# Performance work log

Measured on AMD Instinct MI355X. Metric: run time of the kernel, lower is better.

The kernel has to match this reference:

```python
import jax, jax.numpy as jnp
import numpy as np

N = 50000
E = 800000
IN_C = 256
NHID = 32
HEADS = 4
OUT_C = 64
HID = NHID * HEADS  # 128
SLOPE = 0.2


def setup_inputs() -> dict:
    key = jax.random.key(0)
    ks = jax.random.split(key, 16)
    s = lambda *d: 1.0 / np.sqrt(d[0])
    inp = {
        "x": jax.random.normal(ks[0], (N, IN_C), dtype=jnp.float32),
        "edge_index": jax.random.randint(ks[1], (2, E), 0, N, dtype=jnp.int64),
        # conv1: GATConv(IN_C, NHID, heads=HEADS, concat=True)
        "W1": jax.random.normal(ks[2], (IN_C, HEADS * NHID), dtype=jnp.float32) * s(IN_C),
        "att_src1": jax.random.normal(ks[3], (HEADS, NHID), dtype=jnp.float32) * s(NHID),
        "att_dst1": jax.random.normal(ks[4], (HEADS, NHID), dtype=jnp.float32) * s(NHID),
        "b1": jnp.zeros((HEADS * NHID,), dtype=jnp.float32),
        # conv2: GATConv(HID, OUT_C, heads=1, concat=False)
        "W2": jax.random.normal(ks[5], (HID, OUT_C), dtype=jnp.float32) * s(HID),
        "att_src2": jax.random.normal(ks[6], (1, OUT_C), dtype=jnp.float32) * s(OUT_C),
        "att_dst2": jax.random.normal(ks[7], (1, OUT_C), dtype=jnp.float32) * s(OUT_C),
        "b2": jnp.zeros((OUT_C,), dtype=jnp.float32),
        # res1: Linear(IN_C, HID)
        "res1_w": jax.random.normal(ks[8], (IN_C, HID), dtype=jnp.float32) * s(IN_C),
        "res1_b": jnp.zeros((HID,), dtype=jnp.float32),
        # fc: Linear(HID, OUT_C)
        "fc_w": jax.random.normal(ks[9], (HID, OUT_C), dtype=jnp.float32) * s(HID),
        "fc_b": jnp.zeros((OUT_C,), dtype=jnp.float32),
    }
    return inp


def leaky_relu(x, slope=SLOPE):
    return jnp.where(x >= 0, x, slope * x)


def gat_conv(x, edge_index, W, att_src, att_dst, bias, heads, out_c, concat):
    """PyG GATConv with default add_self_loops=True, negative_slope=0.2."""
    n = x.shape[0]
    loop = jnp.arange(n, dtype=edge_index.dtype)
    src = jnp.concatenate([edge_index[0], loop])  # [E+N]
    dst = jnp.concatenate([edge_index[1], loop])
    h = (x @ W).reshape(n, heads, out_c)          # [N,H,C]
    a_src = (h * att_src[None]).sum(-1)           # [N,H]
    a_dst = (h * att_dst[None]).sum(-1)
    alpha = leaky_relu(a_src[src] + a_dst[dst])   # [E+N,H]
    # segment softmax over destination nodes (every node has a self loop)
    amax = jax.ops.segment_max(alpha, dst, num_segments=n)
    expa = jnp.exp(alpha - amax[dst])
    denom = jax.ops.segment_sum(expa, dst, num_segments=n)
    alpha = expa / (denom[dst] + 1e-16)
    msg = alpha[:, :, None] * h[src]              # [E+N,H,C] irregular gather
    out = jax.ops.segment_sum(msg, dst, num_segments=n)  # scatter-add
    if concat:
        out = out.reshape(n, heads * out_c)
    else:
        out = out.mean(axis=1)
    return out + bias


def reference(x, edge_index, W1, att_src1, att_dst1, b1, W2, att_src2, att_dst2, b2,
              res1_w, res1_b, fc_w, fc_b):
    x_res = x @ res1_w + res1_b
    h = gat_conv(x, edge_index, W1, att_src1, att_dst1, b1, HEADS, NHID, True) + x_res
    h_res = h @ fc_w + fc_b
    h = leaky_relu(h)
    z = gat_conv(h, edge_index, W2, att_src2, att_dst2, b2, 1, OUT_C, False) + h_res
    z = leaky_relu(z)
    return z
```

## Files before the change

### kernel.cpp

```cpp
#include <hip/hip_runtime.h>

typedef __attribute__((ext_vector_type(8))) short short8;
typedef __attribute__((ext_vector_type(4))) float f32x4;

constexpr int BCAP = 4096;

__device__ __forceinline__ ushort rne_bf16(float f) {
  uint u = __float_as_uint(f);
  uint r = (u + 0x7FFFu + ((u >> 16) & 1u)) >> 16;
  return (ushort)r;
}
__device__ __forceinline__ float bf16_lo(uint pair) { return __uint_as_float(pair << 16); }
__device__ __forceinline__ float bf16_hi(uint pair) { return __uint_as_float(pair & 0xffff0000u); }
__device__ __forceinline__ float bf1(ushort v) { return __uint_as_float((uint)v << 16); }
__device__ __forceinline__ float lrelu(float a) { return a >= 0.f ? a : 0.2f * a; }

__device__ __forceinline__ uint lrelu_pair(uint pair) {
  float lo = lrelu(bf16_lo(pair));
  float hi = lrelu(bf16_hi(pair));
  return (uint)rne_bf16(lo) | ((uint)rne_bf16(hi) << 16);
}
__device__ __forceinline__ float4 lrelu_bf8(float4 v) {
  uint4 u = *(uint4*)&v;
  u.x = lrelu_pair(u.x); u.y = lrelu_pair(u.y);
  u.z = lrelu_pair(u.z); u.w = lrelu_pair(u.w);
  return *(float4*)&u;
}
__device__ __forceinline__ float4 pack_bf8(float4 a, float4 b) {
  uint u0 = (uint)rne_bf16(a.x) | ((uint)rne_bf16(a.y) << 16);
  uint u1 = (uint)rne_bf16(a.z) | ((uint)rne_bf16(a.w) << 16);
  uint u2 = (uint)rne_bf16(b.x) | ((uint)rne_bf16(b.y) << 16);
  uint u3 = (uint)rne_bf16(b.z) | ((uint)rne_bf16(b.w) << 16);
  uint4 r; r.x = u0; r.y = u1; r.z = u2; r.w = u3;
  return *(float4*)&r;
}

__global__ __launch_bounds__(256) void prep_all_k(
    const int* __restrict__ ei, int E, int nEB,
    int* __restrict__ bcnt, uint2* __restrict__ tmp, int nbuck,
    const float* __restrict__ W1, const float* __restrict__ res1_w,
    const float* __restrict__ fc_w, const float* __restrict__ W2,
    ushort* __restrict__ Wt1, ushort* __restrict__ fcT, ushort* __restrict__ W2T)
{
  __shared__ int lcnt[400];
  __shared__ int gbase[400];
  const int tid = threadIdx.x, bid = blockIdx.x;
  const long gstride = (long)gridDim.x * 256;
  const long g0 = (long)bid * 256 + tid;

  if (bid < nEB) {
    for (int i = tid; i < nbuck; i += 256) lcnt[i] = 0;
    __syncthreads();
    const int ebase = bid * 4096;
    int srcs[16], dsts[16], rk[16];
#pragma unroll
    for (int i = 0; i < 16; ++i) {
      int e = ebase + i * 256 + tid;
      if (e < E) {
        srcs[i] = ei[e];
        dsts[i] = ei[E + e];
        rk[i] = atomicAdd(&lcnt[dsts[i] >> 7], 1);
      } else dsts[i] = -1;
    }
    __syncthreads();
    for (int b = tid; b < nbuck; b += 256)
      gbase[b] = lcnt[b] ? atomicAdd(&bcnt[b], lcnt[b]) : 0;
    __syncthreads();
#pragma unroll
    for (int i = 0; i < 16; ++i) {
      if (dsts[i] >= 0) {
        int b = dsts[i] >> 7;
        tmp[(size_t)b * BCAP + gbase[b] + rk[i]] = make_uint2((uint)srcs[i], (uint)dsts[i]);
      }
    }
  }

  for (long gi = g0; gi < 81920; gi += gstride) {
    const float* src; ushort* dst; int K, NO; long local;
    if (gi < 32768)            { src = W1;     dst = Wt1;          K = 256; NO = 128; local = gi; }
    else if (gi < 65536)       { src = res1_w; dst = Wt1 + 32768;  K = 256; NO = 128; local = gi - 32768; }
    else if (gi < 65536+8192)  { src = fc_w;   dst = fcT;          K = 128; NO = 64;  local = gi - 65536; }
    else                       { src = W2;     dst = W2T;          K = 128; NO = 64;  local = gi - 65536 - 8192; }
    int n = (int)(local / K), k = (int)(local % K);
    dst[local] = rne_bf16(src[(size_t)k * NO + n]);
  }
}

__global__ __launch_bounds__(512) void scan_buckets_k(const int* __restrict__ bcnt,
                                                      int* __restrict__ bbase,
                                                      int* __restrict__ offp,
                                                      int nbuck, int N) {
  __shared__ int sh[512];
  int tid = threadIdx.x;
  int v = (tid < nbuck) ? bcnt[tid] : 0;
  sh[tid] = v;
  __syncthreads();
  for (int o = 1; o < 512; o <<= 1) {
    int t = (tid >= o) ? sh[tid - o] : 0;
    __syncthreads();
    sh[tid] += t;
    __syncthreads();
  }
  if (tid < nbuck) bbase[tid] = sh[tid] - v;
  if (tid == nbuck - 1) { bbase[nbuck] = sh[tid]; offp[N] = sh[tid]; }
}

__global__ __launch_bounds__(512) void gemm1_k(
    const float* __restrict__ x, const ushort* __restrict__ Wt1,
    const float* __restrict__ res1_b,
    const float* __restrict__ att_s1, const float* __restrict__ att_d1,
    ushort* __restrict__ h1bf, ushort* __restrict__ xresbf,
    float* __restrict__ a_s, float* __restrict__ a_d,
    const uint2* __restrict__ tmp, const int* __restrict__ bcnt,
    const int* __restrict__ bbase, int* __restrict__ offp,
    int* __restrict__ csr, int nbuck, int M)
{
  constexpr int LDA = 72;
  __shared__ ushort smem[64 * LDA + 128 * LDA];
  const int bid = blockIdx.x, y = blockIdx.y, tid = threadIdx.x;
  ushort* As = smem;
  ushort* Bs = smem + 64 * LDA;
  const int w = tid >> 6, l = tid & 63;
  const int wr = w >> 2, wc = w & 3;
  const int l15 = l & 15, lg = l >> 4;
  const int row0 = bid * 64;
  const int srow = tid >> 3, sch = tid & 7;

  int gra = row0 + srow; if (gra >= M) gra = M - 1;
  const float*  Apf = x + (size_t)gra * 256 + sch * 8;
  const ushort* Bp  = Wt1 + ((size_t)y * 128 + srow) * 256 + sch * 8;

  f32x4 acc[2][2] = {};
  float4 raCa, raCb, rbC0, rbC1, raNa, raNb, rbN0, rbN1;
  raCa = *(const float4*)(Apf);
  raCb = *(const float4*)(Apf + 4);
  rbC0 = *(const float4*)(Bp);
  rbC1 = *(const float4*)(Bp + 64 * 256);

#pragma unroll
  for (int kt = 0; kt < 4; ++kt) {
    __syncthreads();
    *(float4*)&As[srow * LDA + sch * 8] = pack_bf8(raCa, raCb);
    *(float4*)&Bs[srow * LDA + sch * 8] = rbC0;
    *(float4*)&Bs[(64 + srow) * LDA + sch * 8] = rbC1;
    __syncthreads();
    if (kt < 3) {
      int k1 = (kt + 1) * 64;
      raNa = *(const float4*)(Apf + k1);
      raNb = *(const float4*)(Apf + k1 + 4);
      rbN0 = *(const float4*)(Bp + k1);
      rbN1 = *(const float4*)(Bp + 64 * 256 + k1);
    }
    short8 aF[2][2], bF[2][2];
#pragma unroll
    for (int m = 0; m < 2; ++m)
#pragma unroll
      for (int kk = 0; kk < 2; ++kk)
        aF[m][kk] = *(const short8*)&As[(wr * 32 + m * 16 + l15) * LDA + kk * 32 + lg * 8];
#pragma unroll
    for (int n = 0; n < 2; ++n)
#pragma unroll
      for (int kk = 0; kk < 2; ++kk)
        bF[n][kk] = *(const short8*)&Bs[(wc * 32 + n * 16 + l15) * LDA + kk * 32 + lg * 8];
#pragma unroll
    for (int m = 0; m < 2; ++m)
#pragma unroll
      for (int n = 0; n < 2; ++n)
#pragma unroll
        for (int kk = 0; kk < 2; ++kk)
          acc[m][n] = __builtin_amdgcn_mfma_f32_16x16x32_bf16(aF[m][kk], bF[n][kk], acc[m][n], 0, 0, 0);
    raCa = raNa; raCb = raNb; rbC0 = rbN0; rbC1 = rbN1;
  }
  __syncthreads();

  ushort* Cs = smem;
#pragma unroll
  for (int m = 0; m < 2; ++m)
#pragma unroll
    for (int n = 0; n < 2; ++n)
#pragma unroll
      for (int j = 0; j < 4; ++j) {
        int rl = wr * 32 + m * 16 + lg * 4 + j;
        int col = wc * 32 + n * 16 + l15;
        float v = acc[m][n][j] + (y ? res1_b[col] : 0.f);
        Cs[rl * 128 + col] = rne_bf16(v);
      }
  __syncthreads();

  if (y == 0) {
    int r = tid >> 3, s = tid & 7, h = s >> 1;
    int gr = row0 + r;
    float ps = 0.f, pd = 0.f;
#pragma unroll
    for (int i = 0; i < 16; ++i) {
      int col = s * 16 + i;
      float v = bf1(Cs[r * 128 + col]);
      ps += v * att_s1[h * 32 + (col & 31)];
      pd += v * att_d1[h * 32 + (col & 31)];
    }
    ps += __shfl_xor(ps, 1, 64);
    pd += __shfl_xor(pd, 1, 64);
    if (!(s & 1) && gr < M) { a_s[gr * 4 + h] = ps; a_d[gr * 4 + h] = pd; }
  }

  {
    ushort* out = y ? xresbf : h1bf;
#pragma unroll
    for (int idx = tid; idx < 1024; idx += 512) {
      int row = idx >> 4, c16 = idx & 15;
      int gr = row0 + row;
      if (gr < M)
        *(uint4*)&out[(size_t)gr * 128 + c16 * 8] = *(const uint4*)&Cs[row * 128 + c16 * 8];
    }
  }

  if (y == 1 && bid < nbuck) {
    __syncthreads();
    int* lcnt = (int*)smem;
    int* excl = lcnt + 128;
    const int vbase = bid * 128;
    const int nloc = ((vbase + 128 < M) ? 128 : M - vbase);
    const int cntb = bcnt[bid];
    const int bbase0 = bbase[bid];
    const uint2* bt = tmp + (size_t)bid * BCAP;
    if (tid < 128) lcnt[tid] = 0;
    __syncthreads();
    for (int e = tid; e < cntb; e += 512)
      atomicAdd(&lcnt[(int)bt[e].y - vbase], 1);
    __syncthreads();
    if (tid < 128) {
      int v = lcnt[tid];
      int sc = v;
#pragma unroll
      for (int o = 1; o < 64; o <<= 1) {
        int t = __shfl_up(sc, o, 64);
        if ((tid & 63) >= o) sc += t;
      }
      excl[tid] = sc - v;
    }
    __syncthreads();
    if (tid >= 64 && tid < 128) excl[tid] += excl[63] + lcnt[63];
    __syncthreads();
    if (tid < nloc) offp[vbase + tid] = bbase0 + excl[tid];
    if (tid < 128) lcnt[tid] = 0;
    __syncthreads();
    for (int e = tid; e < cntb; e += 512) {
      uint2 t = bt[e];
      int li = (int)t.y - vbase;
      int r = atomicAdd(&lcnt[li], 1);
      csr[bbase0 + excl[li] + r] = (int)t.x;
    }
  }
}

__global__ __launch_bounds__(512) void gemm2_k(
    const ushort* __restrict__ hpre,
    const ushort* __restrict__ fcT,
    const float* __restrict__ fc_b,
    const float* __restrict__ att_s2, const float* __restrict__ att_d2,
    ushort* __restrict__ hresb, ushort* __restrict__ h2bf,
    float* __restrict__ a_s, float* __restrict__ a_d, int M)
{
  constexpr int LDA = 72;
  __shared__ ushort smem[64 * LDA + 64 * LDA];
  const int tid = threadIdx.x, y = blockIdx.y;
  const ushort* B = fcT + (size_t)y * 64 * 128;
  ushort* out = y ? h2bf : hresb;
  const int row0 = blockIdx.x * 64;
  ushort* As = smem;
  ushort* Bs = smem + 64 * LDA;
  const int w = tid >> 6, l = tid & 63;
  const int wr = w >> 1, wc = w & 1;
  const int l15 = l & 15, lg = l >> 4;
  const int srow = tid >> 3, sch = tid & 7;

  int gra = row0 + srow; if (gra >= M) gra = M - 1;
  const ushort* Ap = hpre + (size_t)gra * 128 + sch * 8;
  const ushort* Bp = B + (size_t)srow * 128 + sch * 8;

  f32x4 acc[2] = {};
  float4 raC = *(const float4*)(Ap);
  float4 rbC = *(const float4*)(Bp);
  if (y) raC = lrelu_bf8(raC);
  float4 raN, rbN;

#pragma unroll
  for (int kt = 0; kt < 2; ++kt) {
    __syncthreads();
    *(float4*)&As[srow * LDA + sch * 8] = raC;
    *(float4*)&Bs[srow * LDA + sch * 8] = rbC;
    __syncthreads();
    if (kt < 1) {
      raN = *(const float4*)(Ap + 64);
      rbN = *(const float4*)(Bp + 64);
      if (y) raN = lrelu_bf8(raN);
    }

    short8 aF[2], bF[2][2];
#pragma unroll
    for (int kk = 0; kk < 2; ++kk)
      aF[kk] = *(const short8*)&As[(wr * 16 + l15) * LDA + kk * 32 + lg * 8];
#pragma unroll
    for (int n = 0; n < 2; ++n)
#pragma unroll
      for (int kk = 0; kk < 2; ++kk)
        bF[n][kk] = *(const short8*)&Bs[(wc * 32 + n * 16 + l15) * LDA + kk * 32 + lg * 8];
#pragma unroll
    for (int n = 0; n < 2; ++n)
#pragma unroll
      for (int kk = 0; kk < 2; ++kk)
        acc[n] = __builtin_amdgcn_mfma_f32_16x16x32_bf16(aF[kk], bF[n][kk], acc[n], 0, 0, 0);
    raC = raN; rbC = rbN;
  }
  __syncthreads();

  ushort* Cs = smem;
#pragma unroll
  for (int n = 0; n < 2; ++n)
#pragma unroll
    for (int j = 0; j < 4; ++j) {
      int rl = wr * 16 + lg * 4 + j;
      int col = wc * 32 + n * 16 + l15;
      float v = acc[n][j] + (y == 0 ? fc_b[col] : 0.f);
      Cs[rl * 64 + col] = rne_bf16(v);
    }
  __syncthreads();

  if (y == 1) {
    int r = tid >> 3, s = tid & 7;
    int gr = row0 + r;
    float ps = 0.f, pd = 0.f;
#pragma unroll
    for (int i = 0; i < 8; ++i) {
      int col = s * 8 + i;
      float v = bf1(Cs[r * 64 + col]);
      ps += v * att_s2[col];
      pd += v * att_d2[col];
    }
    ps += __shfl_xor(ps, 1, 64); pd += __shfl_xor(pd, 1, 64);
    ps += __shfl_xor(ps, 2, 64); pd += __shfl_xor(pd, 2, 64);
    ps += __shfl_xor(ps, 4, 64); pd += __shfl_xor(pd, 4, 64);
    if (s == 0 && gr < M) { a_s[gr] = ps; a_d[gr] = pd; }
  }

  {
    int row = tid >> 3, c16 = tid & 7;
    int gr = row0 + row;
    if (gr < M)
      *(uint4*)&out[(size_t)gr * 64 + c16 * 8] = *(const uint4*)&Cs[row * 64 + c16 * 8];
  }
}

__global__ __launch_bounds__(256) void aggr1_k(const uint* __restrict__ h1u,
                                               const uint* __restrict__ xresu,
                                               const float* __restrict__ a_s,
                                               const float* __restrict__ a_d,
                                               const int* __restrict__ off,
                                               const int* __restrict__ csr,
                                               const float* __restrict__ b1,
                                               uint* __restrict__ hpreu, int n) {
  int w = threadIdx.x >> 6, l = threadIdx.x & 63;
  int d = blockIdx.x * 4 + w;
  if (d >= n) return;
  int h = l >> 4, c = l * 2;
  int le = l & 15, hb = l & 48;
  float adh = a_d[d * 4 + h];
  float ws = __expf(lrelu(a_s[d * 4 + h] + adh));
  uint pd = h1u[(size_t)d * 64 + l];
  float lsum = ws, accx = ws * bf16_lo(pd), accy = ws * bf16_hi(pd);

  int s0 = off[d], s1 = off[d + 1];
  int p = s0;
  for (; p + 16 <= s1; p += 16) {
    int idxv = csr[p + le];
    float wv = __expf(lrelu(a_s[idxv * 4 + h] + adh));
    float wi[16]; int sv[16];
#pragma unroll
    for (int i = 0; i < 16; ++i) {
      wi[i] = __shfl(wv, hb + i, 64);
      sv[i] = __shfl(idxv, i, 64);
    }
#pragma unroll
    for (int i = 0; i < 16; ++i) {
      uint q = h1u[(size_t)sv[i] * 64 + l];
      lsum += wi[i];
      accx += wi[i] * bf16_lo(q);
      accy += wi[i] * bf16_hi(q);
    }
  }
  if (p < s1) {
    int rem = s1 - p;
    int jp = p + le;
    bool valid = jp < s1;
    int jc = valid ? jp : s1 - 1;
    int idxv = csr[jc];
    float wv = valid ? __expf(lrelu(a_s[idxv * 4 + h] + adh)) : 0.f;
    for (int i = 0; i < rem; i += 4) {
#pragma unroll
      for (int j = 0; j < 4; ++j) {
        float wib = __shfl(wv, hb + i + j, 64);
        int svb = __shfl(idxv, i + j, 64);
        uint q = h1u[(size_t)svb * 64 + l];
        lsum += wib;
        accx += wib * bf16_lo(q);
        accy += wib * bf16_hi(q);
      }
    }
  }
  float inv = 1.f / (lsum + 1e-16f);
  uint xr = xresu[(size_t)d * 64 + l];
  float vx = accx * inv + b1[c] + bf16_lo(xr);
  float vy = accy * inv + b1[c + 1] + bf16_hi(xr);
  hpreu[(size_t)d * 64 + l] = (uint)rne_bf16(vx) | ((uint)rne_bf16(vy) << 16);
}

__global__ __launch_bounds__(256) void aggr2_k(const ushort* __restrict__ h2b,
                                               const ushort* __restrict__ hresb,
                                               const float* __restrict__ a_s,
                                               const float* __restrict__ a_d,
                                               const int* __restrict__ off,
                                               const int* __restrict__ csr,
                                               const float* __restrict__ b2,
                                               float* __restrict__ out, int n) {
  int w = threadIdx.x >> 6, l = threadIdx.x & 63;
  int d = blockIdx.x * 4 + w;
  if (d >= n) return;
  int le = l & 15;
  float adh = a_d[d];
  float ws = __expf(lrelu(a_s[d] + adh));
  float lsum = ws;
  float acc = ws * bf1(h2b[(size_t)d * 64 + l]);

  int s0 = off[d], s1 = off[d + 1];
  int p = s0;
  for (; p + 16 <= s1; p += 16) {
    int idxv = csr[p + le];
    float wv = __expf(lrelu(a_s[idxv] + adh));
    float wi[16]; int sv[16];
#pragma unroll
    for (int i = 0; i < 16; ++i) {
      wi[i] = __shfl(wv, i, 64);
      sv[i] = __shfl(idxv, i, 64);
    }
#pragma unroll
    for (int i = 0; i < 16; ++i) {
      float fv = bf1(h2b[(size_t)sv[i] * 64 + l]);
      lsum += wi[i];
      acc += wi[i] * fv;
    }
  }
  if (p < s1) {
    int rem = s1 - p;
    int jp = p + le;
    bool valid = jp < s1;
    int jc = valid ? jp : s1 - 1;
    int idxv = csr[jc];
    float wv = valid ? __expf(lrelu(a_s[idxv] + adh)) : 0.f;
    for (int i = 0; i < rem; i += 4) {
#pragma unroll
      for (int j = 0; j < 4; ++j) {
        float wib = __shfl(wv, i + j, 64);
        int svb = __shfl(idxv, i + j, 64);
        float fv = bf1(h2b[(size_t)svb * 64 + l]);
        lsum += wib;
        acc += wib * fv;
      }
    }
  }
  float inv = 1.f / (lsum + 1e-16f);
  float z = acc * inv + b2[l] + bf1(hresb[(size_t)d * 64 + l]);
  out[(size_t)d * 64 + l] = lrelu(z);
}

extern "C" void kernel_launch(void* const* d_in, const int* in_sizes, int n_in,
                              void* d_out, int out_size, void* d_ws, size_t ws_size,
                              hipStream_t stream) {
  const float* x        = (const float*)d_in[0];
  const int*   ei       = (const int*)d_in[1];
  const float* W1       = (const float*)d_in[2];
  const float* att_src1 = (const float*)d_in[3];
  const float* att_dst1 = (const float*)d_in[4];
  const float* b1       = (const float*)d_in[5];
  const float* W2       = (const float*)d_in[6];
  const float* att_src2 = (const float*)d_in[7];
  const float* att_dst2 = (const float*)d_in[8];
  const float* b2       = (const float*)d_in[9];
  const float* res1_w   = (const float*)d_in[10];
  const float* res1_b   = (const float*)d_in[11];
  const float* fc_w     = (const float*)d_in[12];
  const float* fc_b     = (const float*)d_in[13];
  float* out = (float*)d_out;

  const int N = in_sizes[0] / 256;
  const int E = in_sizes[1] / 2;
  const int nbuck = (N + 127) / 128;
  const int nEB = (E + 4095) / 4096;

  ushort* h1bf   = (ushort*)d_ws;
  ushort* xresbf = h1bf + (size_t)N * 128;
  uint*   hpreu  = (uint*)(xresbf + (size_t)N * 128);
  float*  as1    = (float*)(hpreu + (size_t)N * 64);
  float*  ad1    = as1 + (size_t)N * 4;
  ushort* Wt1    = (ushort*)(ad1 + (size_t)N * 4);
  ushort* fcT    = Wt1 + 256 * 256;
  ushort* W2T    = fcT + 64 * 128;
  int* offp      = (int*)(W2T + 64 * 128);
  int* csr       = offp + N + 1;
  int* bcnt      = csr + E;
  int* bbase     = bcnt + 512;
  uint2* tmp     = (uint2*)(((uintptr_t)(bbase + 520) + 7) & ~(uintptr_t)7);
  ushort* h2bf   = h1bf;
  ushort* hresb  = xresbf;
  float*  as2 = as1, *ad2 = ad1;

  const int ngemm = (N + 63) / 64;

  hipMemsetAsync(bcnt, 0, 512 * 4, stream);
  prep_all_k<<<nEB, 256, 0, stream>>>(ei, E, nEB, bcnt, tmp, nbuck,
                                      W1, res1_w, fc_w, W2, Wt1, fcT, W2T);
  scan_buckets_k<<<1, 512, 0, stream>>>(bcnt, bbase, offp, nbuck, N);

  gemm1_k<<<dim3(ngemm, 2), 512, 0, stream>>>(x, Wt1, res1_b, att_src1, att_dst1,
                                              h1bf, xresbf, as1, ad1,
                                              tmp, bcnt, bbase, offp, csr, nbuck, N);

  aggr1_k<<<(N + 3) / 4, 256, 0, stream>>>((const uint*)h1bf, (const uint*)xresbf, as1, ad1,
                                           offp, csr, b1, hpreu, N);

  gemm2_k<<<dim3(ngemm, 2), 512, 0, stream>>>(
      (const ushort*)hpreu, fcT, fc_b,
      att_src2, att_dst2, hresb, h2bf, as2, ad2, N);

  aggr2_k<<<(N + 3) / 4, 256, 0, stream>>>(h2bf, hresb, as2, ad2, offp, csr, b2, out, N);
}
```

Baseline: 149.3 us.

## Fuse layer-1 aggregation into second GEMM via shared-memory hpre tile

Merges the layer-1 attention aggregation kernel with the second-layer GEMM. Each 512-thread block aggregates 64 destination nodes into a bf16 tile in shared memory, then runs both the fc and W2 products on that tile with MFMA. This removes the global write and re-read of the intermediate hpre buffer and one kernel launch. In exchange, occupancy for the irregular gather phase drops: 782 large blocks with a bigger shared-memory footprint replace 12500 small ones, and layer-2 outputs now need separate workspace buffers.

```diff
diff --git a/kernel.cpp b/kernel.cpp
--- a/kernel.cpp
+++ b/kernel.cpp
@@ -20,11 +20,11 @@
   float hi = lrelu(bf16_hi(pair));
   return (uint)rne_bf16(lo) | ((uint)rne_bf16(hi) << 16);
 }
-__device__ __forceinline__ float4 lrelu_bf8(float4 v) {
+__device__ __forceinline__ short8 lrelu_s8(short8 v) {
   uint4 u = *(uint4*)&v;
   u.x = lrelu_pair(u.x); u.y = lrelu_pair(u.y);
   u.z = lrelu_pair(u.z); u.w = lrelu_pair(u.w);
-  return *(float4*)&u;
+  return *(short8*)&u;
 }
 __device__ __forceinline__ float4 pack_bf8(float4 a, float4 b) {
   uint u0 = (uint)rne_bf16(a.x) | ((uint)rne_bf16(a.y) << 16);
@@ -253,165 +253,146 @@
   }
 }
 
-__global__ __launch_bounds__(512) void gemm2_k(
-    const ushort* __restrict__ hpre,
+__global__ __launch_bounds__(512) void agg1_gemm2_k(
+    const uint* __restrict__ h1u, const uint* __restrict__ xresu,
+    const float* __restrict__ a_s1, const float* __restrict__ a_d1,
+    const int* __restrict__ off, const int* __restrict__ csr,
+    const float* __restrict__ b1,
     const ushort* __restrict__ fcT,
     const float* __restrict__ fc_b,
     const float* __restrict__ att_s2, const float* __restrict__ att_d2,
     ushort* __restrict__ hresb, ushort* __restrict__ h2bf,
-    float* __restrict__ a_s, float* __restrict__ a_d, int M)
+    float* __restrict__ a_s2, float* __restrict__ a_d2, int n)
 {
-  constexpr int LDA = 72;
-  __shared__ ushort smem[64 * LDA + 64 * LDA];
-  const int tid = threadIdx.x, y = blockIdx.y;
-  const ushort* B = fcT + (size_t)y * 64 * 128;
-  ushort* out = y ? h2bf : hresb;
-  const int row0 = blockIdx.x * 64;
-  ushort* As = smem;
-  ushort* Bs = smem + 64 * LDA;
+  constexpr int LDH = 136;
+  __shared__ ushort smem[64 * LDH + 128 * LDH];
+  ushort* hpreT = smem;
+  ushort* Bs    = smem + 64 * LDH;
+
+  const int tid = threadIdx.x;
   const int w = tid >> 6, l = tid & 63;
-  const int wr = w >> 1, wc = w & 1;
   const int l15 = l & 15, lg = l >> 4;
-  const int srow = tid >> 3, sch = tid & 7;
-
-  int gra = row0 + srow; if (gra >= M) gra = M - 1;
-  const ushort* Ap = hpre + (size_t)gra * 128 + sch * 8;
-  const ushort* Bp = B + (size_t)srow * 128 + sch * 8;
-
-  f32x4 acc[2] = {};
-  float4 raC = *(const float4*)(Ap);
-  float4 rbC = *(const float4*)(Bp);
-  if (y) raC = lrelu_bf8(raC);
-  float4 raN, rbN;
-
-#pragma unroll
-  for (int kt = 0; kt < 2; ++kt) {
-    __syncthreads();
-    *(float4*)&As[srow * LDA + sch * 8] = raC;
-    *(float4*)&Bs[srow * LDA + sch * 8] = rbC;
-    __syncthreads();
-    if (kt < 1) {
-      raN = *(const float4*)(Ap + 64);
-      rbN = *(const float4*)(Bp + 64);
-      if (y) raN = lrelu_bf8(raN);
-    }
-
-    short8 aF[2], bF[2][2];
-#pragma unroll
-    for (int kk = 0; kk < 2; ++kk)
-      aF[kk] = *(const short8*)&As[(wr * 16 + l15) * LDA + kk * 32 + lg * 8];
-#pragma unroll
-    for (int n = 0; n < 2; ++n)
-#pragma unroll
-      for (int kk = 0; kk < 2; ++kk)
-        bF[n][kk] = *(const short8*)&Bs[(wc * 32 + n * 16 + l15) * LDA + kk * 32 + lg * 8];
-#pragma unroll
-    for (int n = 0; n < 2; ++n)
-#pragma unroll
-      for (int kk = 0; kk < 2; ++kk)
-        acc[n] = __builtin_amdgcn_mfma_f32_16x16x32_bf16(aF[kk], bF[n][kk], acc[n], 0, 0, 0);
-    raC = raN; rbC = rbN;
+  const int d0 = blockIdx.x * 64;
+
+#pragma unroll
+  for (int c = tid; c < 2048; c += 512) {
+    int row = c >> 4, ch = c & 15;
+    *(uint4*)&Bs[row * LDH + ch * 8] = *(const uint4*)&fcT[(size_t)row * 128 + ch * 8];
+  }
+
+  const int h = l >> 4, c2 = l * 2;
+  const int le = l & 15, hb = l & 48;
+  for (int k = 0; k < 8; ++k) {
+    int dl = w * 8 + k;
+    int d = d0 + dl;
+    if (d < n) {
+      float adh = a_d1[d * 4 + h];
+      float ws = __expf(lrelu(a_s1[d * 4 + h] + adh));
+      uint pd = h1u[(size_t)d * 64 + l];
+      float lsum = ws, accx = ws * bf16_lo(pd), accy = ws * bf16_hi(pd);
+
+      int s0 = off[d], s1 = off[d + 1];
+      int p = s0;
+      for (; p + 16 <= s1; p += 16) {
+        int idxv = csr[p + le];
+        float wv = __expf(lrelu(a_s1[idxv * 4 + h] + adh));
+        float wi[16]; int sv[16];
+#pragma unroll
+        for (int i = 0; i < 16; ++i) {
+          wi[i] = __shfl(wv, hb + i, 64);
+          sv[i] = __shfl(idxv, i, 64);
+        }
+#pragma unroll
+        for (int i = 0; i < 16; ++i) {
+          uint q = h1u[(size_t)sv[i] * 64 + l];
+          lsum += wi[i];
+          accx += wi[i] * bf16_lo(q);
+          accy += wi[i] * bf16_hi(q);
+        }
+      }
+      if (p < s1) {
+        int rem = s1 - p;
+        int jp = p + le;
+        bool valid = jp < s1;
+        int jc = valid ? jp : s1 - 1;
+        int idxv = csr[jc];
+        float wv = valid ? __expf(lrelu(a_s1[idxv * 4 + h] + adh)) : 0.f;
+        for (int i = 0; i < rem; i += 4) {
+#pragma unroll
+          for (int j = 0; j < 4; ++j) {
+            float wib = __shfl(wv, hb + i + j, 64);
+            int svb = __shfl(idxv, i + j, 64);
+            uint q = h1u[(size_t)svb * 64 + l];
+            lsum += wib;
+            accx += wib * bf16_lo(q);
+            accy += wib * bf16_hi(q);
+          }
+        }
+      }
+      float inv = 1.f / (lsum + 1e-16f);
+      uint xr = xresu[(size_t)d * 64 + l];
+      float vx = accx * inv + b1[c2] + bf16_lo(xr);
+      float vy = accy * inv + b1[c2 + 1] + bf16_hi(xr);
+      *(uint*)&hpreT[dl * LDH + c2] = (uint)rne_bf16(vx) | ((uint)rne_bf16(vy) << 16);
+    } else if (dl < 64) {
+      *(uint*)&hpreT[dl * LDH + c2] = 0;
+    }
   }
   __syncthreads();
 
-  ushort* Cs = smem;
-#pragma unroll
-  for (int n = 0; n < 2; ++n)
+  const int yh = w >> 2;
+  const int wr = w & 3;
+  f32x4 acc[4] = {};
+#pragma unroll
+  for (int kk = 0; kk < 4; ++kk) {
+    short8 aF = *(const short8*)&hpreT[(wr * 16 + l15) * LDH + kk * 32 + lg * 8];
+    if (yh) aF = lrelu_s8(aF);
+#pragma unroll
+    for (int nn = 0; nn < 4; ++nn) {
+      short8 bF = *(const short8*)&Bs[(yh * 64 + nn * 16 + l15) * LDH + kk * 32 + lg * 8];
+      acc[nn] = __builtin_amdgcn_mfma_f32_16x16x32_bf16(aF, bF, acc[nn], 0, 0, 0);
+    }
+  }
+  __syncthreads();
+
+  ushort* C0 = smem;
+  ushort* C1 = smem + 4096;
+#pragma unroll
+  for (int nn = 0; nn < 4; ++nn)
 #pragma unroll
     for (int j = 0; j < 4; ++j) {
       int rl = wr * 16 + lg * 4 + j;
-      int col = wc * 32 + n * 16 + l15;
-      float v = acc[n][j] + (y == 0 ? fc_b[col] : 0.f);
-      Cs[rl * 64 + col] = rne_bf16(v);
+      int col = nn * 16 + l15;
+      float v = acc[nn][j] + (yh == 0 ? fc_b[col] : 0.f);
+      (yh ? C1 : C0)[rl * 64 + col] = rne_bf16(v);
     }
   __syncthreads();
 
-  if (y == 1) {
+  {
     int r = tid >> 3, s = tid & 7;
-    int gr = row0 + r;
-    float ps = 0.f, pd = 0.f;
+    int d = d0 + r;
+    float ps = 0.f, pdd = 0.f;
 #pragma unroll
     for (int i = 0; i < 8; ++i) {
       int col = s * 8 + i;
-      float v = bf1(Cs[r * 64 + col]);
+      float v = bf1(C1[r * 64 + col]);
       ps += v * att_s2[col];
-      pd += v * att_d2[col];
-    }
-    ps += __shfl_xor(ps, 1, 64); pd += __shfl_xor(pd, 1, 64);
-    ps += __shfl_xor(ps, 2, 64); pd += __shfl_xor(pd, 2, 64);
-    ps += __shfl_xor(ps, 4, 64); pd += __shfl_xor(pd, 4, 64);
-    if (s == 0 && gr < M) { a_s[gr] = ps; a_d[gr] = pd; }
+      pdd += v * att_d2[col];
+    }
+    ps += __shfl_xor(ps, 1, 64); pdd += __shfl_xor(pdd, 1, 64);
+    ps += __shfl_xor(ps, 2, 64); pdd += __shfl_xor(pdd, 2, 64);
+    ps += __shfl_xor(ps, 4, 64); pdd += __shfl_xor(pdd, 4, 64);
+    if (s == 0 && d < n) { a_s2[d] = ps; a_d2[d] = pdd; }
   }
 
   {
-    int row = tid >> 3, c16 = tid & 7;
-    int gr = row0 + row;
-    if (gr < M)
-      *(uint4*)&out[(size_t)gr * 64 + c16 * 8] = *(const uint4*)&Cs[row * 64 + c16 * 8];
-  }
-}
-
-__global__ __launch_bounds__(256) void aggr1_k(const uint* __restrict__ h1u,
-                                               const uint* __restrict__ xresu,
-                                               const float* __restrict__ a_s,
-                                               const float* __restrict__ a_d,
-                                               const int* __restrict__ off,
-                                               const int* __restrict__ csr,
-                                               const float* __restrict__ b1,
-                                               uint* __restrict__ hpreu, int n) {
-  int w = threadIdx.x >> 6, l = threadIdx.x & 63;
-  int d = blockIdx.x * 4 + w;
-  if (d >= n) return;
-  int h = l >> 4, c = l * 2;
-  int le = l & 15, hb = l & 48;
-  float adh = a_d[d * 4 + h];
-  float ws = __expf(lrelu(a_s[d * 4 + h] + adh));
-  uint pd = h1u[(size_t)d * 64 + l];
-  float lsum = ws, accx = ws * bf16_lo(pd), accy = ws * bf16_hi(pd);
-
-  int s0 = off[d], s1 = off[d + 1];
-  int p = s0;
-  for (; p + 16 <= s1; p += 16) {
-    int idxv = csr[p + le];
-    float wv = __expf(lrelu(a_s[idxv * 4 + h] + adh));
-    float wi[16]; int sv[16];
-#pragma unroll
-    for (int i = 0; i < 16; ++i) {
-      wi[i] = __shfl(wv, hb + i, 64);
-      sv[i] = __shfl(idxv, i, 64);
-    }
-#pragma unroll
-    for (int i = 0; i < 16; ++i) {
-      uint q = h1u[(size_t)sv[i] * 64 + l];
-      lsum += wi[i];
-      accx += wi[i] * bf16_lo(q);
-      accy += wi[i] * bf16_hi(q);
-    }
-  }
-  if (p < s1) {
-    int rem = s1 - p;
-    int jp = p + le;
-    bool valid = jp < s1;
-    int jc = valid ? jp : s1 - 1;
-    int idxv = csr[jc];
-    float wv = valid ? __expf(lrelu(a_s[idxv * 4 + h] + adh)) : 0.f;
-    for (int i = 0; i < rem; i += 4) {
-#pragma unroll
-      for (int j = 0; j < 4; ++j) {
-        float wib = __shfl(wv, hb + i + j, 64);
-        int svb = __shfl(idxv, i + j, 64);
-        uint q = h1u[(size_t)svb * 64 + l];
-        lsum += wib;
-        accx += wib * bf16_lo(q);
-        accy += wib * bf16_hi(q);
-      }
-    }
-  }
-  float inv = 1.f / (lsum + 1e-16f);
-  uint xr = xresu[(size_t)d * 64 + l];
-  float vx = accx * inv + b1[c] + bf16_lo(xr);
-  float vy = accy * inv + b1[c + 1] + bf16_hi(xr);
-  hpreu[(size_t)d * 64 + l] = (uint)rne_bf16(vx) | ((uint)rne_bf16(vy) << 16);
+    int row = tid >> 3, ch = tid & 7;
+    int d = d0 + row;
+    if (d < n) {
+      *(uint4*)&hresb[(size_t)d * 64 + ch * 8] = *(const uint4*)&C0[row * 64 + ch * 8];
+      *(uint4*)&h2bf[(size_t)d * 64 + ch * 8]  = *(const uint4*)&C1[row * 64 + ch * 8];
+    }
+  }
 }
 
 __global__ __launch_bounds__(256) void aggr2_k(const ushort* __restrict__ h2b,
@@ -498,10 +479,13 @@
 
   ushort* h1bf   = (ushort*)d_ws;
   ushort* xresbf = h1bf + (size_t)N * 128;
-  uint*   hpreu  = (uint*)(xresbf + (size_t)N * 128);
-  float*  as1    = (float*)(hpreu + (size_t)N * 64);
+  ushort* hresb  = xresbf + (size_t)N * 128;
+  ushort* h2bf   = hresb + (size_t)N * 64;
+  float*  as1    = (float*)(h2bf + (size_t)N * 64);
   float*  ad1    = as1 + (size_t)N * 4;
-  ushort* Wt1    = (ushort*)(ad1 + (size_t)N * 4);
+  float*  as2    = ad1 + (size_t)N * 4;
+  float*  ad2    = as2 + (size_t)N;
+  ushort* Wt1    = (ushort*)(ad2 + (size_t)N);
   ushort* fcT    = Wt1 + 256 * 256;
   ushort* W2T    = fcT + 64 * 128;
   int* offp      = (int*)(W2T + 64 * 128);
@@ -509,9 +493,6 @@
   int* bcnt      = csr + E;
   int* bbase     = bcnt + 512;
   uint2* tmp     = (uint2*)(((uintptr_t)(bbase + 520) + 7) & ~(uintptr_t)7);
-  ushort* h2bf   = h1bf;
-  ushort* hresb  = xresbf;
-  float*  as2 = as1, *ad2 = ad1;
 
   const int ngemm = (N + 63) / 64;
 
@@ -524,12 +505,9 @@
                                               h1bf, xresbf, as1, ad1,
                                               tmp, bcnt, bbase, offp, csr, nbuck, N);
 
-  aggr1_k<<<(N + 3) / 4, 256, 0, stream>>>((const uint*)h1bf, (const uint*)xresbf, as1, ad1,
-                                           offp, csr, b1, hpreu, N);
-
-  gemm2_k<<<dim3(ngemm, 2), 512, 0, stream>>>(
-      (const ushort*)hpreu, fcT, fc_b,
-      att_src2, att_dst2, hresb, h2bf, as2, ad2, N);
+  agg1_gemm2_k<<<ngemm, 512, 0, stream>>>(
+      (const uint*)h1bf, (const uint*)xresbf, as1, ad1, offp, csr, b1,
+      fcT, fc_b, att_src2, att_dst2, hresb, h2bf, as2, ad2, N);
 
   aggr2_k<<<(N + 3) / 4, 256, 0, stream>>>(h2bf, hresb, as2, ad2, offp, csr, b2, out, N);
 }
```

Result: slower. 166.7 us (+11.6%).
